# Performance work log

Measured on AMD Instinct MI355X. Metric: run time of the kernel, lower is better.

## Reference

```python
import jax, jax.numpy as jnp
import numpy as np
from jax import lax

B_, L_, D_, N_, K_ = 2, 4096, 1024, 16, 4


def setup_inputs() -> dict:
    key = jax.random.key(0)
    ks = jax.random.split(key, 11)
    s = lambda fan: 1.0 / np.sqrt(fan)
    return {
        "x": jax.random.normal(ks[0], (B_, L_, D_), jnp.float32),
        "W_in": jax.random.normal(ks[1], (D_, 2 * D_), jnp.float32) * s(D_),
        "b_in": jax.random.normal(ks[2], (2 * D_,), jnp.float32) * 0.01,
        "conv_w": jax.random.normal(ks[3], (D_, K_), jnp.float32) * s(K_),
        "conv_b": jax.random.normal(ks[4], (D_,), jnp.float32) * 0.01,
        "W_x": jax.random.normal(ks[5], (D_, 2 * N_), jnp.float32) * s(D_),
        "b_x": jax.random.normal(ks[6], (2 * N_,), jnp.float32) * 0.01,
        "A_log": jax.random.normal(ks[7], (D_, N_), jnp.float32),
        "D_param": jnp.ones((D_,), jnp.float32),
        "W_out": jax.random.normal(ks[8], (D_, D_), jnp.float32) * s(D_),
        "b_out": jax.random.normal(ks[9], (D_,), jnp.float32) * 0.01,
    }


def silu(x):
    return x * jax.nn.sigmoid(x)


def s6_forward(x, W_in, b_in, conv_w, conv_b, W_x, b_x, A_log, D_param, W_out, b_out):
    b, L, D = x.shape
    # in_proj then split into ssm stream and gate
    x_and_gate = x @ W_in + b_in                      # [b, L, 2D]
    x_ssm, gate = jnp.split(x_and_gate, 2, axis=-1)   # each [b, L, D]

    # depthwise causal conv: padding=(d_conv-1, d_conv-1) then [:, :, :L] == left-pad only
    xc = jnp.transpose(x_ssm, (0, 2, 1))              # [b, D, L]
    xc = lax.conv_general_dilated(
        xc, conv_w[:, None, :],                       # [D, 1, K]
        window_strides=(1,), padding=[(K_ - 1, 0)],
        feature_group_count=D,
        dimension_numbers=("NCH", "OIH", "NCH"),
    ) + conv_b[None, :, None]
    x_conv = silu(jnp.transpose(xc, (0, 2, 1)))       # [b, L, D]

    # data-dependent B, C
    BC = x_conv @ W_x + b_x                           # [b, L, 2N]
    B_mat, C_mat = jnp.split(BC, 2, axis=-1)          # each [b, L, N]

    A_discrete = jnp.exp(-jnp.exp(A_log))             # [D, N]

    # sequential selective scan over L, carry h: [b, D, N]
    def step(h, inp):
        xc_t, B_t, C_t = inp                          # [b,D], [b,N], [b,N]
        h = A_discrete[None] * h + xc_t[:, :, None] * B_t[:, None, :]
        y = jnp.einsum("bn,bdn->bd", C_t, h) + D_param * xc_t
        return h, y

    h0 = jnp.zeros((b, D, N_), x.dtype)
    xs = (jnp.transpose(x_conv, (1, 0, 2)),
          jnp.transpose(B_mat, (1, 0, 2)),
          jnp.transpose(C_mat, (1, 0, 2)))
    h_final, ys = lax.scan(step, h0, xs)              # ys: [L, b, D]
    y = jnp.transpose(ys, (1, 0, 2))                  # [b, L, D]

    y = y * silu(gate)
    y = y @ W_out + b_out
    final_state = h_final.mean(axis=1)                # [b, N]
    return y, final_state


def reference(x, W_in, b_in, conv_w, conv_b, W_x, b_x, A_log, D_param, W_out, b_out):
    return s6_forward(x, W_in, b_in, conv_w, conv_b, W_x, b_x, A_log, D_param, W_out, b_out)
```

## Files before the change

### kernel.cpp

```cpp
#include <hip/hip_runtime.h>
#include <hip/hip_bf16.h>
#include <math.h>

#define LL 4096
#define DD 1024
#define NN 16
#define KK 4
#define BB 2
#define MM (BB * LL)
#define NC 64
#define LC 64

typedef unsigned short ushort_t;
typedef short s16x8 __attribute__((ext_vector_type(8)));
typedef float f32x4 __attribute__((ext_vector_type(4)));
typedef unsigned int u32;

__device__ __forceinline__ ushort_t f2bf(float f) {
  __hip_bfloat16 h = __float2bfloat16(f);
  return *reinterpret_cast<ushort_t*>(&h);
}
__device__ __forceinline__ float bf2f(ushort_t u) {
  union { u32 i; float f; } c;
  c.i = ((u32)u) << 16;
  return c.f;
}

template <bool BF16OUT>
__global__ __launch_bounds__(256) void gemm_bt_mfma(
    const ushort_t* __restrict__ A,
    const ushort_t* __restrict__ BT,
    const float* __restrict__ bias,
    void* __restrict__ Cv, int N) {
  constexpr int K = 1024;
  __shared__ ushort_t As[128 * 32];
  __shared__ ushort_t Bs[128 * 32];

  const int tid = threadIdx.x;
  const int lane = tid & 63;
  const int w = tid >> 6;
  const int wm = w & 1, wn = w >> 1;
  const int row0 = blockIdx.y * 128;
  const int col0 = blockIdx.x * 128;

  const int lrow = lane >> 2;
  const int lk = (lane & 3) * 8;

  f32x4 acc[4][4];
#pragma unroll
  for (int i = 0; i < 4; ++i)
#pragma unroll
    for (int j = 0; j < 4; ++j) acc[i][j] = (f32x4){0.f, 0.f, 0.f, 0.f};

  const int frow = lane & 15;
  const int quad = lane >> 4;

  for (int k0 = 0; k0 < K; k0 += 32) {
#pragma unroll
    for (int it = 0; it < 2; ++it) {
      int r = it * 64 + w * 16;
      __builtin_amdgcn_global_load_lds(
          (const __attribute__((address_space(1))) u32*)(A + (size_t)(row0 + r + lrow) * K + k0 + lk),
          (__attribute__((address_space(3))) u32*)(As + r * 32), 16, 0, 0);
      __builtin_amdgcn_global_load_lds(
          (const __attribute__((address_space(1))) u32*)(BT + (size_t)(col0 + r + lrow) * K + k0 + lk),
          (__attribute__((address_space(3))) u32*)(Bs + r * 32), 16, 0, 0);
    }
    __syncthreads();

    s16x8 af[4], bf[4];
#pragma unroll
    for (int mi = 0; mi < 4; ++mi)
      af[mi] = *(const s16x8*)&As[(wm * 64 + mi * 16 + frow) * 32 + quad * 8];
#pragma unroll
    for (int ni = 0; ni < 4; ++ni)
      bf[ni] = *(const s16x8*)&Bs[(wn * 64 + ni * 16 + frow) * 32 + quad * 8];
#pragma unroll
    for (int mi = 0; mi < 4; ++mi)
#pragma unroll
      for (int ni = 0; ni < 4; ++ni)
        acc[mi][ni] = __builtin_amdgcn_mfma_f32_16x16x32_bf16(
            af[mi], bf[ni], acc[mi][ni], 0, 0, 0);
    __syncthreads();
  }

#pragma unroll
  for (int mi = 0; mi < 4; ++mi) {
#pragma unroll
    for (int ni = 0; ni < 4; ++ni) {
      int col = col0 + wn * 64 + ni * 16 + frow;
      float b = bias[col];
#pragma unroll
      for (int r = 0; r < 4; ++r) {
        int row = row0 + wm * 64 + mi * 16 + quad * 4 + r;
        if constexpr (BF16OUT)
          ((ushort_t*)Cv)[(size_t)row * N + col] = f2bf(acc[mi][ni][r] + b);
        else
          ((float*)Cv)[(size_t)row * N + col] = acc[mi][ni][r] + b;
      }
    }
  }
}

__global__ __launch_bounds__(128) void bc_mfma_k(
    const ushort_t* __restrict__ A,
    const ushort_t* __restrict__ BT,
    const float* __restrict__ bias,
    float* __restrict__ C) {
  constexpr int K = 1024;
  __shared__ ushort_t As[32 * 32];
  __shared__ ushort_t Bs[32 * 32];

  const int tid = threadIdx.x;
  const int lane = tid & 63;
  const int w = tid >> 6;
  const int row0 = blockIdx.x * 32;
  const int lrow = lane >> 2;
  const int lk = (lane & 3) * 8;
  const int frow = lane & 15;
  const int quad = lane >> 4;

  f32x4 acc[2];
  acc[0] = (f32x4){0.f, 0.f, 0.f, 0.f};
  acc[1] = (f32x4){0.f, 0.f, 0.f, 0.f};

  for (int k0 = 0; k0 < K; k0 += 32) {
    __builtin_amdgcn_global_load_lds(
        (const __attribute__((address_space(1))) u32*)(A + (size_t)(row0 + w * 16 + lrow) * K + k0 + lk),
        (__attribute__((address_space(3))) u32*)(As + (w * 16) * 32), 16, 0, 0);
    __builtin_amdgcn_global_load_lds(
        (const __attribute__((address_space(1))) u32*)(BT + (size_t)(w * 16 + lrow) * K + k0 + lk),
        (__attribute__((address_space(3))) u32*)(Bs + (w * 16) * 32), 16, 0, 0);
    __syncthreads();

    s16x8 af = *(const s16x8*)&As[(w * 16 + frow) * 32 + quad * 8];
    s16x8 bf0 = *(const s16x8*)&Bs[(frow)*32 + quad * 8];
    s16x8 bf1 = *(const s16x8*)&Bs[(16 + frow) * 32 + quad * 8];
    acc[0] = __builtin_amdgcn_mfma_f32_16x16x32_bf16(af, bf0, acc[0], 0, 0, 0);
    acc[1] = __builtin_amdgcn_mfma_f32_16x16x32_bf16(af, bf1, acc[1], 0, 0, 0);
    __syncthreads();
  }

#pragma unroll
  for (int ni = 0; ni < 2; ++ni) {
    int col = ni * 16 + frow;
    float b = bias[col];
#pragma unroll
    for (int r = 0; r < 4; ++r) {
      int row = row0 + w * 16 + quad * 4 + r;
      C[(size_t)row * 32 + col] = acc[ni][r] + b;
    }
  }
}

__global__ __launch_bounds__(256) void cast_bf16_k(
    const float* __restrict__ src, ushort_t* __restrict__ dst,
    float* __restrict__ fs) {
  if (blockIdx.x == 0 && threadIdx.x < 32) fs[threadIdx.x] = 0.f;
  int i = blockIdx.x * 256 + threadIdx.x;
  float4 v = ((const float4*)src)[i];
  ushort4 o;
  o.x = f2bf(v.x); o.y = f2bf(v.y); o.z = f2bf(v.z); o.w = f2bf(v.w);
  ((ushort4*)dst)[i] = o;
}

__global__ void transpose_cast3_k(
    const float* __restrict__ W_in, const float* __restrict__ W_out,
    const float* __restrict__ W_x, ushort_t* __restrict__ WinT,
    ushort_t* __restrict__ WoutT, ushort_t* __restrict__ WxT) {
  constexpr int K = 1024;
  const float* W;
  ushort_t* WT;
  int N;
  if (blockIdx.z == 0) {
    W = W_in; WT = WinT; N = 2048;
  } else if (blockIdx.z == 1) {
    if (blockIdx.x >= 32) return;
    W = W_out; WT = WoutT; N = 1024;
  } else {
    if (blockIdx.x >= 1) return;
    W = W_x; WT = WxT; N = 32;
  }
  __shared__ float t[32][33];
  int nb = blockIdx.x * 32, kb = blockIdx.y * 32;
  int tx = threadIdx.x, ty = threadIdx.y;
#pragma unroll
  for (int i = 0; i < 32; i += 8)
    t[ty + i][tx] = W[(size_t)(kb + ty + i) * N + nb + tx];
  __syncthreads();
#pragma unroll
  for (int i = 0; i < 32; i += 8)
    WT[(size_t)(nb + ty + i) * K + kb + tx] = f2bf(t[tx][ty + i]);
}

__global__ __launch_bounds__(256) void conv_silu_k(
    const ushort_t* __restrict__ XGb, const float* __restrict__ conv_w,
    const float* __restrict__ conv_b, ushort_t* __restrict__ XCb) {
  __shared__ float cw[128 * 33];
  const int tid = threadIdx.x;
#pragma unroll
  for (int j = 0; j < 4; ++j) {
    int d = tid + j * 256;
    float4 v = ((const float4*)conv_w)[d];
    float* p = &cw[(d >> 3) * 33 + (d & 7) * 4];
    p[0] = v.x; p[1] = v.y; p[2] = v.z; p[3] = v.w;
  }
  __syncthreads();

  int gid = blockIdx.x * 256 + tid;
  int m = gid >> 7;
  int dg = gid & 127;
  int d0 = dg * 8;
  int l = m & (LL - 1);
  const float* w = &cw[dg * 33];

  float4 b0 = ((const float4*)conv_b)[dg * 2];
  float4 b1 = ((const float4*)conv_b)[dg * 2 + 1];
  float acc[8] = {b0.x, b0.y, b0.z, b0.w, b1.x, b1.y, b1.z, b1.w};

#pragma unroll
  for (int k = 0; k < KK; ++k) {
    int li = l + k - (KK - 1);
    if (li < 0) continue;
    s16x8 v = *(const s16x8*)(XGb + (size_t)(m + k - (KK - 1)) * 2048 + d0);
#pragma unroll
    for (int j = 0; j < 8; ++j)
      acc[j] += bf2f((ushort_t)v[j]) * w[j * 4 + k];
  }
  ushort_t o[8];
#pragma unroll
  for (int j = 0; j < 8; ++j) {
    float s = acc[j] / (1.f + __expf(-acc[j]));
    o[j] = f2bf(s);
  }
  *(s16x8*)(XCb + (size_t)m * DD + d0) = *(const s16x8*)o;
}

__global__ __launch_bounds__(64) void scan_local_k(
    const ushort_t* __restrict__ XCb, const float* __restrict__ BC,
    const float* __restrict__ A_log, float* __restrict__ S) {
  const int b = blockIdx.x, c = blockIdx.y;
  const int tid = threadIdx.x;
  const int d0 = blockIdx.z * 128 + tid * 2;
  const int t0 = c * LC;
  const size_t rowb = (size_t)b * LL;

  __shared__ float bcs[LC * 32];
  {
    const float4* src = (const float4*)(BC + (rowb + t0) * 32);
    float4* dst = (float4*)bcs;
#pragma unroll
    for (int i = 0; i < 8; ++i) dst[tid + i * 64] = src[tid + i * 64];
  }

  float a0[NN], a1[NN], h0[NN], h1[NN];
#pragma unroll
  for (int n = 0; n < NN; ++n) {
    a0[n] = expf(-expf(A_log[d0 * NN + n]));
    a1[n] = expf(-expf(A_log[(d0 + 1) * NN + n]));
    h0[n] = 0.f;
    h1[n] = 0.f;
  }
  __syncthreads();

  const ushort_t* xp = XCb + (rowb + t0) * DD + d0;
  u32 xw = *(const u32*)xp;
  for (int t = 0; t < LC; ++t) {
    u32 xw_n = (t + 1 < LC) ? *(const u32*)(xp + (size_t)(t + 1) * DD) : 0u;
    float x0 = bf2f((ushort_t)(xw & 0xffff));
    float x1 = bf2f((ushort_t)(xw >> 16));
    const float* bp = bcs + t * 32;
#pragma unroll
    for (int n = 0; n < NN; ++n) {
      float bv = bp[n];
      h0[n] = a0[n] * h0[n] + x0 * bv;
      h1[n] = a1[n] * h1[n] + x1 * bv;
    }
    xw = xw_n;
  }
  float* sp = S + (((size_t)(b * NC + c)) * DD + d0) * NN;
#pragma unroll
  for (int n = 0; n < NN; ++n) sp[n] = h0[n];
#pragma unroll
  for (int n = 0; n < NN; ++n) sp[NN + n] = h1[n];
}

__global__ __launch_bounds__(256) void scan_carry_k(
    float* __restrict__ S, const float* __restrict__ A_log,
    float* __restrict__ fs) {
  const int idx = blockIdx.x * 256 + threadIdx.x;
  const int n = idx & (NN - 1);
  const int d = (idx / NN) & (DD - 1);
  const int b = idx / (NN * DD);

  const float aLC = expf(-(float)LC * expf(A_log[d * NN + n]));
  float h = 0.f;
  for (int c = 0; c < NC; ++c) {
    size_t off = (((size_t)(b * NC + c)) * DD + d) * NN + n;
    float s = S[off];
    S[off] = h;
    h = aLC * h + s;
  }
  __shared__ float red[256];
  red[threadIdx.x] = h * (1.f / (float)DD);
  __syncthreads();
  if (threadIdx.x < NN) {
    float sum = 0.f;
#pragma unroll
    for (int i = 0; i < 16; ++i) sum += red[i * NN + threadIdx.x];
    atomicAdd(&fs[b * NN + threadIdx.x], sum);
  }
}

__global__ __launch_bounds__(64) void scan_final_k(
    const ushort_t* __restrict__ XCb, const ushort_t* __restrict__ XGb,
    const float* __restrict__ BC, const float* __restrict__ A_log,
    const float* __restrict__ D_param, const float* __restrict__ H0,
    ushort_t* __restrict__ Y1b) {
  const int b = blockIdx.x, c = blockIdx.y;
  const int tid = threadIdx.x;
  const int d0 = blockIdx.z * 128 + tid * 2;
  const int t0 = c * LC;
  const size_t rowb = (size_t)b * LL;

  __shared__ float bcs[LC * 32];
  {
    const float4* src = (const float4*)(BC + (rowb + t0) * 32);
    float4* dst = (float4*)bcs;
#pragma unroll
    for (int i = 0; i < 8; ++i) dst[tid + i * 64] = src[tid + i * 64];
  }

  float a0[NN], a1[NN], h0[NN], h1[NN];
  const float* hp = H0 + (((size_t)(b * NC + c)) * DD + d0) * NN;
#pragma unroll
  for (int n = 0; n < NN; ++n) {
    a0[n] = expf(-expf(A_log[d0 * NN + n]));
    a1[n] = expf(-expf(A_log[(d0 + 1) * NN + n]));
    h0[n] = hp[n];
    h1[n] = hp[NN + n];
  }
  const float Dp0 = D_param[d0], Dp1 = D_param[d0 + 1];
  __syncthreads();

  const ushort_t* xp = XCb + (rowb + t0) * DD + d0;
  const ushort_t* gp = XGb + (rowb + t0) * 2048 + DD + d0;
  ushort_t* yp = Y1b + (rowb + t0) * DD + d0;
  u32 xw = *(const u32*)xp;
  u32 gw = *(const u32*)gp;
  for (int t = 0; t < LC; ++t) {
    u32 xw_n = 0u, gw_n = 0u;
    if (t + 1 < LC) {
      xw_n = *(const u32*)(xp + (size_t)(t + 1) * DD);
      gw_n = *(const u32*)(gp + (size_t)(t + 1) * 2048);
    }
    float x0 = bf2f((ushort_t)(xw & 0xffff));
    float x1 = bf2f((ushort_t)(xw >> 16));
    float g0 = bf2f((ushort_t)(gw & 0xffff));
    float g1 = bf2f((ushort_t)(gw >> 16));
    float y0 = Dp0 * x0, y1 = Dp1 * x1;
    const float* bp = bcs + t * 32;
#pragma unroll
    for (int n = 0; n < NN; ++n) {
      float bv = bp[n], cv = bp[16 + n];
      h0[n] = a0[n] * h0[n] + x0 * bv;
      h1[n] = a1[n] * h1[n] + x1 * bv;
      y0 += cv * h0[n];
      y1 += cv * h1[n];
    }
    float sg0 = g0 / (1.f + __expf(-g0));
    float sg1 = g1 / (1.f + __expf(-g1));
    u32 outw = (u32)f2bf(y0 * sg0) | ((u32)f2bf(y1 * sg1) << 16);
    *(u32*)(yp + (size_t)t * DD) = outw;
    xw = xw_n;
    gw = gw_n;
  }
}

extern "C" void kernel_launch(void* const* d_in, const int* in_sizes, int n_in,
                              void* d_out, int out_size, void* d_ws,
                              size_t ws_size, hipStream_t stream) {
  const float* x = (const float*)d_in[0];
  const float* W_in = (const float*)d_in[1];
  const float* b_in = (const float*)d_in[2];
  const float* conv_w = (const float*)d_in[3];
  const float* conv_b = (const float*)d_in[4];
  const float* W_x = (const float*)d_in[5];
  const float* b_x = (const float*)d_in[6];
  const float* A_log = (const float*)d_in[7];
  const float* D_param = (const float*)d_in[8];
  const float* W_out = (const float*)d_in[9];
  const float* b_out = (const float*)d_in[10];
  float* out = (float*)d_out;
  float* fs = out + (size_t)MM * DD;

  float* BC = (float*)d_ws;
  float* S = BC + (size_t)MM * 32;
  ushort_t* Xb = (ushort_t*)(S + (size_t)BB * NC * DD * NN);
  ushort_t* XGb = Xb + (size_t)MM * DD;
  ushort_t* XCb = XGb + (size_t)MM * 2048;
  ushort_t* Y1b = XCb + (size_t)MM * DD;
  ushort_t* WinT = Y1b + (size_t)MM * DD;
  ushort_t* WoutT = WinT + (size_t)2048 * DD;
  ushort_t* WxT = WoutT + (size_t)DD * DD;

  dim3 blk(256);
  cast_bf16_k<<<dim3((MM * DD) / 1024), blk, 0, stream>>>(x, Xb, fs);
  transpose_cast3_k<<<dim3(64, 32, 3), dim3(32, 8), 0, stream>>>(
      W_in, W_out, W_x, WinT, WoutT, WxT);
  gemm_bt_mfma<true><<<dim3(2048 / 128, MM / 128), blk, 0, stream>>>(
      Xb, WinT, b_in, XGb, 2048);
  conv_silu_k<<<dim3((MM * 128) / 256), blk, 0, stream>>>(XGb, conv_w, conv_b,
                                                          XCb);
  bc_mfma_k<<<dim3(MM / 32), dim3(128), 0, stream>>>(XCb, WxT, b_x, BC);
  scan_local_k<<<dim3(BB, NC, DD / 128), dim3(64), 0, stream>>>(XCb, BC, A_log,
                                                                S);
  scan_carry_k<<<dim3((BB * DD * NN) / 256), blk, 0, stream>>>(S, A_log, fs);
  scan_final_k<<<dim3(BB, NC, DD / 128), dim3(64), 0, stream>>>(
      XCb, XGb, BC, A_log, D_param, S, Y1b);
  gemm_bt_mfma<false><<<dim3(1024 / 128, MM / 128), blk, 0, stream>>>(
      Y1b, WoutT, b_out, out, 1024);
}
```

Before: 278.9 us.

## Swizzle GEMM LDS tiles, group block order for L2 reuse, fuse prep kernels

Applies an XOR swizzle to the 16-byte k-chunks stored in LDS in both MFMA GEMM kernels, so fragment reads from different rows land in different banks. The 2D grid is replaced by a 1D grid that walks column tiles in groups of eight per row band, aiming for better L2 reuse of the weight tiles. The input bf16 cast and the weight transpose-casts are merged into a single launch to save one kernel launch. The prep grid contains many blocks that return immediately, and the remapped index math adds a little work per block.

```diff
diff --git a/kernel.cpp b/kernel.cpp
--- a/kernel.cpp
+++ b/kernel.cpp
@@ -40,11 +40,16 @@
   const int lane = tid & 63;
   const int w = tid >> 6;
   const int wm = w & 1, wn = w >> 1;
-  const int row0 = blockIdx.y * 128;
-  const int col0 = blockIdx.x * 128;
+
+  const int GY = MM / 128;
+  const int bid = blockIdx.x;
+  const int group = bid / (8 * GY);
+  const int rem = bid % (8 * GY);
+  const int row0 = (rem / 8) * 128;
+  const int col0 = (group * 8 + (rem & 7)) * 128;
 
   const int lrow = lane >> 2;
-  const int lk = (lane & 3) * 8;
+  const int lkc = (lane & 3) ^ ((lrow >> 1) & 3);
 
   f32x4 acc[4][4];
 #pragma unroll
@@ -54,16 +59,17 @@
 
   const int frow = lane & 15;
   const int quad = lane >> 4;
+  const int sw = (frow >> 1) & 3;
 
   for (int k0 = 0; k0 < K; k0 += 32) {
 #pragma unroll
     for (int it = 0; it < 2; ++it) {
       int r = it * 64 + w * 16;
       __builtin_amdgcn_global_load_lds(
-          (const __attribute__((address_space(1))) u32*)(A + (size_t)(row0 + r + lrow) * K + k0 + lk),
+          (const __attribute__((address_space(1))) u32*)(A + (size_t)(row0 + r + lrow) * K + k0 + lkc * 8),
           (__attribute__((address_space(3))) u32*)(As + r * 32), 16, 0, 0);
       __builtin_amdgcn_global_load_lds(
-          (const __attribute__((address_space(1))) u32*)(BT + (size_t)(col0 + r + lrow) * K + k0 + lk),
+          (const __attribute__((address_space(1))) u32*)(BT + (size_t)(col0 + r + lrow) * K + k0 + lkc * 8),
           (__attribute__((address_space(3))) u32*)(Bs + r * 32), 16, 0, 0);
     }
     __syncthreads();
@@ -71,10 +77,10 @@
     s16x8 af[4], bf[4];
 #pragma unroll
     for (int mi = 0; mi < 4; ++mi)
-      af[mi] = *(const s16x8*)&As[(wm * 64 + mi * 16 + frow) * 32 + quad * 8];
+      af[mi] = *(const s16x8*)&As[(wm * 64 + mi * 16 + frow) * 32 + (quad ^ sw) * 8];
 #pragma unroll
     for (int ni = 0; ni < 4; ++ni)
-      bf[ni] = *(const s16x8*)&Bs[(wn * 64 + ni * 16 + frow) * 32 + quad * 8];
+      bf[ni] = *(const s16x8*)&Bs[(wn * 64 + ni * 16 + frow) * 32 + (quad ^ sw) * 8];
 #pragma unroll
     for (int mi = 0; mi < 4; ++mi)
 #pragma unroll
@@ -116,9 +122,10 @@
   const int w = tid >> 6;
   const int row0 = blockIdx.x * 32;
   const int lrow = lane >> 2;
-  const int lk = (lane & 3) * 8;
+  const int lkc = (lane & 3) ^ ((lrow >> 1) & 3);
   const int frow = lane & 15;
   const int quad = lane >> 4;
+  const int sw = (frow >> 1) & 3;
 
   f32x4 acc[2];
   acc[0] = (f32x4){0.f, 0.f, 0.f, 0.f};
@@ -126,16 +133,16 @@
 
   for (int k0 = 0; k0 < K; k0 += 32) {
     __builtin_amdgcn_global_load_lds(
-        (const __attribute__((address_space(1))) u32*)(A + (size_t)(row0 + w * 16 + lrow) * K + k0 + lk),
+        (const __attribute__((address_space(1))) u32*)(A + (size_t)(row0 + w * 16 + lrow) * K + k0 + lkc * 8),
         (__attribute__((address_space(3))) u32*)(As + (w * 16) * 32), 16, 0, 0);
     __builtin_amdgcn_global_load_lds(
-        (const __attribute__((address_space(1))) u32*)(BT + (size_t)(w * 16 + lrow) * K + k0 + lk),
+        (const __attribute__((address_space(1))) u32*)(BT + (size_t)(w * 16 + lrow) * K + k0 + lkc * 8),
         (__attribute__((address_space(3))) u32*)(Bs + (w * 16) * 32), 16, 0, 0);
     __syncthreads();
 
-    s16x8 af = *(const s16x8*)&As[(w * 16 + frow) * 32 + quad * 8];
-    s16x8 bf0 = *(const s16x8*)&Bs[(frow)*32 + quad * 8];
-    s16x8 bf1 = *(const s16x8*)&Bs[(16 + frow) * 32 + quad * 8];
+    s16x8 af = *(const s16x8*)&As[(w * 16 + frow) * 32 + (quad ^ sw) * 8];
+    s16x8 bf0 = *(const s16x8*)&Bs[(frow)*32 + (quad ^ sw) * 8];
+    s16x8 bf1 = *(const s16x8*)&Bs[(16 + frow) * 32 + (quad ^ sw) * 8];
     acc[0] = __builtin_amdgcn_mfma_f32_16x16x32_bf16(af, bf0, acc[0], 0, 0, 0);
     acc[1] = __builtin_amdgcn_mfma_f32_16x16x32_bf16(af, bf1, acc[1], 0, 0, 0);
     __syncthreads();
@@ -153,37 +160,43 @@
   }
 }
 
-__global__ __launch_bounds__(256) void cast_bf16_k(
-    const float* __restrict__ src, ushort_t* __restrict__ dst,
-    float* __restrict__ fs) {
-  if (blockIdx.x == 0 && threadIdx.x < 32) fs[threadIdx.x] = 0.f;
-  int i = blockIdx.x * 256 + threadIdx.x;
-  float4 v = ((const float4*)src)[i];
-  ushort4 o;
-  o.x = f2bf(v.x); o.y = f2bf(v.y); o.z = f2bf(v.z); o.w = f2bf(v.w);
-  ((ushort4*)dst)[i] = o;
-}
-
-__global__ void transpose_cast3_k(
-    const float* __restrict__ W_in, const float* __restrict__ W_out,
-    const float* __restrict__ W_x, ushort_t* __restrict__ WinT,
-    ushort_t* __restrict__ WoutT, ushort_t* __restrict__ WxT) {
+__global__ __launch_bounds__(256) void prep_k(
+    const float* __restrict__ x, ushort_t* __restrict__ Xb,
+    float* __restrict__ fs, const float* __restrict__ W_in,
+    const float* __restrict__ W_out, const float* __restrict__ W_x,
+    ushort_t* __restrict__ WinT, ushort_t* __restrict__ WoutT,
+    ushort_t* __restrict__ WxT) {
   constexpr int K = 1024;
+  const int tid = threadIdx.x;
+  if (blockIdx.z == 0) {
+    if (blockIdx.x == 0 && blockIdx.y == 0 && tid < 32) fs[tid] = 0.f;
+    int i = (blockIdx.y * 64 + blockIdx.x) * 256 + tid;
+    float4 v = ((const float4*)x)[i];
+    ushort4 o;
+    o.x = f2bf(v.x); o.y = f2bf(v.y); o.z = f2bf(v.z); o.w = f2bf(v.w);
+    ((ushort4*)Xb)[i] = o;
+    return;
+  }
   const float* W;
   ushort_t* WT;
   int N;
-  if (blockIdx.z == 0) {
+  int by = blockIdx.y;
+  if (by < 32) {
     W = W_in; WT = WinT; N = 2048;
-  } else if (blockIdx.z == 1) {
+  } else if (by < 64) {
     if (blockIdx.x >= 32) return;
     W = W_out; WT = WoutT; N = 1024;
-  } else {
+    by -= 32;
+  } else if (by < 96) {
     if (blockIdx.x >= 1) return;
     W = W_x; WT = WxT; N = 32;
+    by -= 64;
+  } else {
+    return;
   }
   __shared__ float t[32][33];
-  int nb = blockIdx.x * 32, kb = blockIdx.y * 32;
-  int tx = threadIdx.x, ty = threadIdx.y;
+  int nb = blockIdx.x * 32, kb = by * 32;
+  int tx = tid & 31, ty = tid >> 5;
 #pragma unroll
   for (int i = 0; i < 32; i += 8)
     t[ty + i][tx] = W[(size_t)(kb + ty + i) * N + nb + tx];
@@ -405,10 +418,9 @@
   ushort_t* WxT = WoutT + (size_t)DD * DD;
 
   dim3 blk(256);
-  cast_bf16_k<<<dim3((MM * DD) / 1024), blk, 0, stream>>>(x, Xb, fs);
-  transpose_cast3_k<<<dim3(64, 32, 3), dim3(32, 8), 0, stream>>>(
-      W_in, W_out, W_x, WinT, WoutT, WxT);
-  gemm_bt_mfma<true><<<dim3(2048 / 128, MM / 128), blk, 0, stream>>>(
+  prep_k<<<dim3(64, 128, 2), blk, 0, stream>>>(x, Xb, fs, W_in, W_out, W_x,
+                                               WinT, WoutT, WxT);
+  gemm_bt_mfma<true><<<dim3((2048 / 128) * (MM / 128)), blk, 0, stream>>>(
       Xb, WinT, b_in, XGb, 2048);
   conv_silu_k<<<dim3((MM * 128) / 256), blk, 0, stream>>>(XGb, conv_w, conv_b,
                                                           XCb);
@@ -418,6 +430,6 @@
   scan_carry_k<<<dim3((BB * DD * NN) / 256), blk, 0, stream>>>(S, A_log, fs);
   scan_final_k<<<dim3(BB, NC, DD / 128), dim3(64), 0, stream>>>(
       XCb, XGb, BC, A_log, D_param, S, Y1b);
-  gemm_bt_mfma<false><<<dim3(1024 / 128, MM / 128), blk, 0, stream>>>(
+  gemm_bt_mfma<false><<<dim3((1024 / 128) * (MM / 128)), blk, 0, stream>>>(
       Y1b, WoutT, b_out, out, 1024);
 }
```

Result: no change. 280.8 us (+0.7%).
